# Kernel optimization log

Hardware: AMD Instinct MI355X
Metric: run time of the kernel (lower is better)

## Reference

```python
import jax, jax.numpy as jnp
import numpy as np

SLOPE = 0.01  # torch LeakyReLU default negative_slope

def _leaky(v):
    return jnp.where(v >= 0, v, SLOPE * v)

def _conv3d(x, w, b, stride):
    y = jax.lax.conv_general_dilated(
        x, w, window_strides=(stride, stride, stride), padding='VALID',
        dimension_numbers=('NCDHW', 'OIDHW', 'NCDHW'))
    return y + b[None, :, None, None, None]

def setup_inputs() -> dict:
    key = jax.random.key(0)
    ks = jax.random.split(key, 12)
    s = 0.05  # small init scale to keep exp(L1) numerically sane
    x = jax.random.normal(ks[0], (64, 1, 92, 92, 92), dtype=jnp.float32)
    w1 = jax.random.normal(ks[1], (16, 1, 6, 6, 6), dtype=jnp.float32) * s
    b1 = jnp.zeros((16,), jnp.float32)
    w2 = jax.random.normal(ks[2], (32, 16, 5, 5, 5), dtype=jnp.float32) * s
    b2 = jnp.zeros((32,), jnp.float32)
    w3 = jax.random.normal(ks[3], (48, 32, 5, 5, 5), dtype=jnp.float32) * s
    b3 = jnp.zeros((48,), jnp.float32)
    w4 = jax.random.normal(ks[4], (64, 48, 3, 3, 3), dtype=jnp.float32) * s
    b4 = jnp.zeros((64,), jnp.float32)
    T = jax.random.normal(ks[5], (512, 64 * 16), dtype=jnp.float32) * s
    Wm = jax.random.normal(ks[6], (512 + 64, 1), dtype=jnp.float32) * s
    bm = jnp.zeros((1,), jnp.float32)
    return {'x': x, 'w1': w1, 'b1': b1, 'w2': w2, 'b2': b2, 'w3': w3,
            'b3': b3, 'w4': w4, 'b4': b4, 'T': T, 'Wm': Wm, 'bm': bm}

def reference(x, w1, b1, w2, b2, w3, b3, w4, b4, T, Wm, bm):
    h = _leaky(_conv3d(x, w1, b1, 2))   # [N,16,44,44,44]
    h = _leaky(_conv3d(h, w2, b2, 3))   # [N,32,14,14,14]
    h = _leaky(_conv3d(h, w3, b3, 3))   # [N,48,4,4,4]
    h = _leaky(_conv3d(h, w4, b4, 1))   # [N,64,2,2,2]
    feature = h.reshape(h.shape[0], -1)  # [N,512]
    # minibatch discrimination: M [N,64,16]
    M = (feature @ T).reshape(-1, 64, 16)
    # pairwise L1 over last dim -> [N,N,64]; sum_j exp(.) -> [N,64]
    dist = jnp.sum(jnp.abs(M[:, None, :, :] - M[None, :, :, :]), axis=-1)
    out_T = jnp.sum(jnp.exp(dist), axis=1)
    z = jnp.concatenate([feature, out_T], axis=1) @ Wm + bm
    return jax.nn.sigmoid(z)
```

## Files before the change

kernel.cpp:

```cpp
#include <hip/hip_runtime.h>
#include <hip/hip_bf16.h>
#include <hip/hip_fp16.h>

typedef _Float16 v2h __attribute__((ext_vector_type(2)));
typedef _Float16 v8h __attribute__((ext_vector_type(8)));
typedef __fp16  v2hf __attribute__((ext_vector_type(2)));
typedef float v4f __attribute__((ext_vector_type(4)));

static inline __device__ float leaky(float v) { return v >= 0.f ? v : 0.01f * v; }

static inline __device__ v2h pkrtz(float a, float b) {
    v2hf r = __builtin_amdgcn_cvt_pkrtz(a, b);
    return __builtin_bit_cast(v2h, r);
}

#define W4T_OFF   0
#define H3_OFF    1655808
#define FEAT_OFF  1852416
#define M_OFF     1885184
#define OT_OFF    1950720
#define F16_BASE  1954816
#define WL1_OFF   0
#define BF2_OFF   4608
#define BF3_OFF   81408
#define H2C_OFF   273408
#define H1C_OFF   5893120

__global__ void prep_kernel(const float* __restrict__ w1, const float* __restrict__ w2,
                            const float* __restrict__ w3, const float* __restrict__ w4,
                            float* __restrict__ w4t, _Float16* __restrict__ Bw1,
                            _Float16* __restrict__ Bf2, _Float16* __restrict__ Bf3) {
    int i = blockIdx.x * 256 + threadIdx.x;
    if (i < 4608) {
        int ks = i >> 9, l = (i >> 3) & 63, j = i & 7;
        int oc = l & 15, kg = l >> 4;
        int g = ks * 4 + kg;
        int kz = g / 6, ky = g % 6;
        Bw1[i] = (j < 6) ? (_Float16)w1[oc * 216 + kz * 36 + ky * 6 + j]
                         : (_Float16)0.f;
    } else if (i < 4608 + 76800) {
        int j2 = i - 4608;
        int nt = j2 / 38400, r = j2 % 38400;
        int t = r / 512, l = (r % 512) >> 3, j = r & 7;
        int oc = nt * 16 + (l & 15);
        int k = (l >> 4) * 8 + j;
        int kz = t / 15, ky = (t % 15) / 3, kxp = t % 3;
        int kx = kxp * 2 + (k >= 16 ? 1 : 0);
        int ic = k & 15;
        Bf2[j2] = (kx < 5) ? (_Float16)w2[oc * 2000 + ic * 125 + kz * 25 + ky * 5 + kx]
                           : (_Float16)0.f;
    } else if (i < 4608 + 76800 + 192000) {
        int j3 = i - (4608 + 76800);
        int nt = j3 / 64000, r = j3 % 64000;
        int tap = r / 512, l = (r % 512) >> 3, j = r & 7;
        int oc = nt * 16 + (l & 15);
        int ic = (l >> 4) * 8 + j;
        Bf3[j3] = (_Float16)w3[oc * 4000 + ic * 125 + tap];
    } else {
        int j4 = i - (4608 + 76800 + 192000);
        if (j4 < 82944) {
            int oc = j4 & 63, t = j4 >> 6;
            w4t[j4] = w4[oc * 1296 + t];
        }
    }
}

__global__ __launch_bounds__(256, 2) void conv1_kernel(
    const float* __restrict__ x, const _Float16* __restrict__ Bw1,
    const float* __restrict__ b1, _Float16* __restrict__ h1c, int n0, int NT) {
    __shared__ __align__(16) _Float16 buf[2][13824];
    int tid = threadIdx.x;
    int lane = tid & 63, wv = tid >> 6;
    int col = lane & 15, kg = lane >> 4;

    int t0 = blockIdx.x;
    if (t0 >= NT) return;

    int D_[13], W_[13];
    bool act_[13];
#pragma unroll
    for (int i = 0; i < 13; i++) {
        int u = tid + i * 256;
        act_[i] = (u < 3312);
        int uu = act_[i] ? u : 0;
        int row = uu / 23, c = uu % 23;
        D_[i] = (row / 12) * 8464 + (row % 12) * 92 + 4 * c;
        W_[i] = row * 96 + 4 * c;
    }

    v8h Bv[9];
#pragma unroll
    for (int ks = 0; ks < 9; ks++) Bv[ks] = *(const v8h*)(Bw1 + ks * 512 + lane * 8);
    int offs[9];
#pragma unroll
    for (int ks = 0; ks < 9; ks++) {
        int g = ks * 4 + kg;
        offs[ks] = ((g / 6) * 12 + (g % 6)) * 192;
    }
    float bias = b1[col];

    if (tid < 144) {
        uint2 zz; zz.x = 0u; zz.y = 0u;
        *(uint2*)(&buf[0][tid * 96 + 92]) = zz;
        *(uint2*)(&buf[1][tid * 96 + 92]) = zz;
    }

    {
        int nb = t0 / 121, rr = t0 % 121;
        const float* bp = x + (long)(n0 + nb) * 778688 + (rr / 11) * 8 * 8464 + (rr % 11) * 8 * 92;
        float4 ld[13];
#pragma unroll
        for (int i = 0; i < 13; i++) if (act_[i]) ld[i] = *(const float4*)(bp + D_[i]);
#pragma unroll
        for (int i = 0; i < 13; i++) if (act_[i]) {
            union { v2h h[2]; uint2 u2; } pk;
            pk.h[0] = pkrtz(ld[i].x, ld[i].y);
            pk.h[1] = pkrtz(ld[i].z, ld[i].w);
            *(uint2*)(&buf[0][W_[i]]) = pk.u2;
        }
    }
    __syncthreads();

    int cur = 0;
    int stride = gridDim.x;
    for (int t = t0; t < NT; t += stride) {
        int tn = t + stride;
        bool hn = tn < NT;
        float4 ld[13];
        if (hn) {
            int nb = tn / 121, rr = tn % 121;
            const float* bp = x + (long)(n0 + nb) * 778688 + (rr / 11) * 8 * 8464 + (rr % 11) * 8 * 92;
#pragma unroll
            for (int i = 0; i < 13; i++) if (act_[i]) ld[i] = *(const float4*)(bp + D_[i]);
        }
        __builtin_amdgcn_sched_barrier(0);

        {
            int nb = t / 121, rr = t % 121;
            int zq = rr / 11, yt = rr % 11;
            const uint* lds32 = (const uint*)&buf[cur][0];
            int z = zq * 4 + wv;
            for (int yy = 0; yy < 4; yy++) {
#pragma unroll
                for (int xt = 0; xt < 3; xt++) {
                    int xo_base = (xt == 2) ? 28 : (xt << 4);
                    int base_byte = (24 * wv + 2 * yy) * 192 + (xo_base + col) * 4;
                    v4f acc = {0.f, 0.f, 0.f, 0.f};
#pragma unroll
                    for (int ks = 0; ks < 9; ks++) {
                        int di = (base_byte + offs[ks]) >> 2;
                        union { uint u[4]; v8h h; } A;
                        A.u[0] = lds32[di + 0];
                        A.u[1] = lds32[di + 1];
                        A.u[2] = lds32[di + 2];
                        A.u[3] = lds32[di + 3];
                        acc = __builtin_amdgcn_mfma_f32_16x16x32_f16(A.h, Bv[ks], acc, 0, 0, 0);
                    }
                    int y = yt * 4 + yy;
                    long obase = ((long)((nb * 44 + z) * 44 + y) * 44 + xo_base + kg * 4) * 16 + col;
#pragma unroll
                    for (int reg = 0; reg < 4; reg++) {
                        h1c[obase + reg * 16] = (_Float16)leaky(acc[reg] + bias);
                    }
                }
            }
        }

        if (hn) {
            _Float16* wb = &buf[cur ^ 1][0];
#pragma unroll
            for (int i = 0; i < 13; i++) if (act_[i]) {
                union { v2h h[2]; uint2 u2; } pk;
                pk.h[0] = pkrtz(ld[i].x, ld[i].y);
                pk.h[1] = pkrtz(ld[i].z, ld[i].w);
                *(uint2*)(wb + W_[i]) = pk.u2;
            }
        }
        __syncthreads();
        cur ^= 1;
    }
}

__global__ __launch_bounds__(256) void conv2_kernel(
    const _Float16* __restrict__ h1c, const _Float16* __restrict__ Bf2,
    const float* __restrict__ b2, _Float16* __restrict__ h2c, int n0, int mlimit) {
    int tid = threadIdx.x;
    int lane = tid & 63, wv = tid >> 6;
    int nwg = gridDim.x;
    int orig = blockIdx.x;
    int xcd = orig & 7, lid = orig >> 3;
    int q = nwg >> 3, r = nwg & 7;
    int swz = (xcd < r ? xcd * (q + 1) : r * (q + 1) + (xcd - r) * q) + lid;
    int t0 = (swz * 4 + wv) * 4;
    int col = lane & 15, kgrp = lane >> 4;
    int par = kgrp >> 1, ico = (kgrp & 1) * 8;

    int base[4];
    bool valid[4];
#pragma unroll
    for (int i = 0; i < 4; i++) {
        int m = (t0 + i) * 16 + col;
        valid[i] = m < mlimit;
        int mm = valid[i] ? m : 0;
        int nl = mm / 2744, rm = mm % 2744;
        int z = rm / 196; rm %= 196;
        int y = rm / 14, xx = rm % 14;
        base[i] = nl * 1362944 + z * 3 * 30976 + y * 3 * 704 + xx * 3 * 16 + ico + par * 16;
    }

    v4f acc[4][2];
#pragma unroll
    for (int i = 0; i < 4; i++)
#pragma unroll
        for (int nt = 0; nt < 2; nt++) acc[i][nt] = (v4f){0.f, 0.f, 0.f, 0.f};

    int t = 0;
    for (int kz = 0; kz < 5; kz++) {
        for (int ky = 0; ky < 5; ky++) {
#pragma unroll
            for (int kxp = 0; kxp < 3; kxp++, t++) {
                int d = kz * 30976 + ky * 704 + kxp * 32;
                v8h B0 = *(const v8h*)(Bf2 + t * 512 + lane * 8);
                v8h B1 = *(const v8h*)(Bf2 + (75 + t) * 512 + lane * 8);
                v8h A0 = *(const v8h*)(h1c + base[0] + d);
                v8h A1 = *(const v8h*)(h1c + base[1] + d);
                v8h A2 = *(const v8h*)(h1c + base[2] + d);
                v8h A3 = *(const v8h*)(h1c + base[3] + d);
                acc[0][0] = __builtin_amdgcn_mfma_f32_16x16x32_f16(A0, B0, acc[0][0], 0, 0, 0);
                acc[0][1] = __builtin_amdgcn_mfma_f32_16x16x32_f16(A0, B1, acc[0][1], 0, 0, 0);
                acc[1][0] = __builtin_amdgcn_mfma_f32_16x16x32_f16(A1, B0, acc[1][0], 0, 0, 0);
                acc[1][1] = __builtin_amdgcn_mfma_f32_16x16x32_f16(A1, B1, acc[1][1], 0, 0, 0);
                acc[2][0] = __builtin_amdgcn_mfma_f32_16x16x32_f16(A2, B0, acc[2][0], 0, 0, 0);
                acc[2][1] = __builtin_amdgcn_mfma_f32_16x16x32_f16(A2, B1, acc[2][1], 0, 0, 0);
                acc[3][0] = __builtin_amdgcn_mfma_f32_16x16x32_f16(A3, B0, acc[3][0], 0, 0, 0);
                acc[3][1] = __builtin_amdgcn_mfma_f32_16x16x32_f16(A3, B1, acc[3][1], 0, 0, 0);
            }
        }
    }

#pragma unroll
    for (int i = 0; i < 4; i++) {
        if (!valid[i]) continue;
#pragma unroll
        for (int nt = 0; nt < 2; nt++) {
            int oc = nt * 16 + col;
            float bb = b2[oc];
#pragma unroll
            for (int reg = 0; reg < 4; reg++) {
                int mlocal = (t0 + i) * 16 + kgrp * 4 + reg;
                float vv = leaky(acc[i][nt][reg] + bb);
                h2c[(long)(n0 * 2744 + mlocal) * 32 + oc] = (_Float16)vv;
            }
        }
    }
}

__global__ __launch_bounds__(256) void conv3_kernel(
    const _Float16* __restrict__ h2c, const _Float16* __restrict__ Bf3,
    const float* __restrict__ b3, float* __restrict__ h3) {
    __shared__ float part[3][64][13];
    int tid = threadIdx.x;
    int lane = tid & 63, wv = tid >> 6;
    int mt = blockIdx.x;
    int col = lane & 15, kgrp = lane >> 4;
    int m = mt * 16 + col;
    int n = m >> 6, pos = m & 63;
    int z = pos >> 4, y = (pos >> 2) & 3, xx = pos & 3;
    int base = (n * 2744 + z * 3 * 196 + y * 3 * 14 + xx * 3) * 32 + kgrp * 8;

    v4f acc[3];
#pragma unroll
    for (int nt = 0; nt < 3; nt++) acc[nt] = (v4f){0.f, 0.f, 0.f, 0.f};

    int tap0 = wv * 32;
    int tap1 = tap0 + 32 < 125 ? tap0 + 32 : 125;
    for (int tap = tap0; tap < tap1; tap++) {
        int kz = tap / 25, rr = tap % 25, ky = rr / 5, kx = rr % 5;
        int d = (kz * 196 + ky * 14 + kx) * 32;
        v8h A  = *(const v8h*)(h2c + base + d);
        v8h B0 = *(const v8h*)(Bf3 + tap * 512 + lane * 8);
        v8h B1 = *(const v8h*)(Bf3 + (125 + tap) * 512 + lane * 8);
        v8h B2 = *(const v8h*)(Bf3 + (250 + tap) * 512 + lane * 8);
        acc[0] = __builtin_amdgcn_mfma_f32_16x16x32_f16(A, B0, acc[0], 0, 0, 0);
        acc[1] = __builtin_amdgcn_mfma_f32_16x16x32_f16(A, B1, acc[1], 0, 0, 0);
        acc[2] = __builtin_amdgcn_mfma_f32_16x16x32_f16(A, B2, acc[2], 0, 0, 0);
    }

    if (wv > 0) {
#pragma unroll
        for (int nt = 0; nt < 3; nt++)
#pragma unroll
            for (int reg = 0; reg < 4; reg++)
                part[wv - 1][lane][nt * 4 + reg] = acc[nt][reg];
    }
    __syncthreads();
    if (wv == 0) {
#pragma unroll
        for (int w = 0; w < 3; w++)
#pragma unroll
            for (int nt = 0; nt < 3; nt++)
#pragma unroll
                for (int reg = 0; reg < 4; reg++)
                    acc[nt][reg] += part[w][lane][nt * 4 + reg];
#pragma unroll
        for (int nt = 0; nt < 3; nt++) {
            int oc = nt * 16 + col;
            float bb = b3[oc];
#pragma unroll
            for (int reg = 0; reg < 4; reg++) {
                int md = mt * 16 + kgrp * 4 + reg;
                h3[((md >> 6) * 48 + oc) * 64 + (md & 63)] = leaky(acc[nt][reg] + bb);
            }
        }
    }
}

__global__ void conv4_kernel(const float* __restrict__ h3, const float* __restrict__ w4t,
                             const float* __restrict__ b4, float* __restrict__ feat) {
    int o = blockIdx.x * 128 + threadIdx.x;
    int pos = o & 7;
    int oc  = (o >> 3) & 63;
    int n   = o >> 9;
    int px = pos & 1, py = (pos >> 1) & 1, pz = pos >> 2;
    const float* xn = h3 + (long)n * 48 * 64;
    float acc = 0.f;
    for (int ic = 0; ic < 48; ic++) {
        const float* xc = xn + ic * 64;
        int tb = ic * 27;
#pragma unroll
        for (int kz = 0; kz < 3; kz++)
#pragma unroll
            for (int ky = 0; ky < 3; ky++)
#pragma unroll
                for (int kx = 0; kx < 3; kx++) {
                    float v = xc[(pz + kz) * 16 + (py + ky) * 4 + (px + kx)];
                    acc += v * w4t[(tb + (kz * 3 + ky) * 3 + kx) * 64 + oc];
                }
    }
    feat[o] = leaky(acc + b4[oc]);
}

__global__ void m_kernel(const float* __restrict__ feat, const float* __restrict__ T,
                         float* __restrict__ M) {
    int o = blockIdx.x * 256 + threadIdx.x;
    int col = o & 1023;
    int n   = o >> 10;
    const float* fr = feat + n * 512;
    float acc = 0.f;
#pragma unroll 4
    for (int f = 0; f < 512; f++) acc += fr[f] * T[f * 1024 + col];
    M[o] = acc;
}

__global__ void outt_kernel(const float* __restrict__ M, float* __restrict__ oT) {
    __shared__ float part[3][64];
    int i = blockIdx.x;
    int tid = threadIdx.x;
    int k = tid & 63, jq = tid >> 6;
    float mi[16];
    const float4* Mi = (const float4*)(M + i * 1024 + k * 16);
#pragma unroll
    for (int q = 0; q < 4; q++) {
        float4 a = Mi[q];
        mi[q*4+0] = a.x; mi[q*4+1] = a.y; mi[q*4+2] = a.z; mi[q*4+3] = a.w;
    }
    float s = 0.f;
    for (int j = jq * 16; j < jq * 16 + 16; j++) {
        const float4* Mj = (const float4*)(M + j * 1024 + k * 16);
        float d = 0.f;
#pragma unroll
        for (int q = 0; q < 4; q++) {
            float4 a = Mj[q];
            d += fabsf(mi[q*4+0]-a.x) + fabsf(mi[q*4+1]-a.y) + fabsf(mi[q*4+2]-a.z) + fabsf(mi[q*4+3]-a.w);
        }
        s += __expf(d);
    }
    if (jq > 0) part[jq - 1][k] = s;
    __syncthreads();
    if (jq == 0) {
        s += part[0][k] + part[1][k] + part[2][k];
        oT[i * 64 + k] = s;
    }
}

__global__ void final_kernel(const float* __restrict__ feat, const float* __restrict__ oT,
                             const float* __restrict__ Wm, const float* __restrict__ bm,
                             float* __restrict__ out) {
    int i = blockIdx.x;
    int lane = threadIdx.x;
    const float* fr = feat + i * 512;
    float z = 0.f;
#pragma unroll
    for (int q = 0; q < 8; q++) z += fr[lane + q * 64] * Wm[lane + q * 64];
    z += oT[i * 64 + lane] * Wm[512 + lane];
#pragma unroll
    for (int off = 32; off > 0; off >>= 1) z += __shfl_down(z, off);
    if (lane == 0) out[i] = 1.f / (1.f + __expf(-(z + bm[0])));
}

extern "C" void kernel_launch(void* const* d_in, const int* in_sizes, int n_in,
                              void* d_out, int out_size, void* d_ws, size_t ws_size,
                              hipStream_t stream) {
    const float* x  = (const float*)d_in[0];
    const float* w1 = (const float*)d_in[1];
    const float* b1 = (const float*)d_in[2];
    const float* w2 = (const float*)d_in[3];
    const float* b2 = (const float*)d_in[4];
    const float* w3 = (const float*)d_in[5];
    const float* b3 = (const float*)d_in[6];
    const float* w4 = (const float*)d_in[7];
    const float* b4 = (const float*)d_in[8];
    const float* T  = (const float*)d_in[9];
    const float* Wm = (const float*)d_in[10];
    const float* bm = (const float*)d_in[11];

    float* ws   = (float*)d_ws;
    float* w4t  = ws + W4T_OFF;
    float* h3   = ws + H3_OFF;
    float* feat = ws + FEAT_OFF;
    float* Mb   = ws + M_OFF;
    float* oT   = ws + OT_OFF;
    _Float16* f16b = (_Float16*)(ws + F16_BASE);
    _Float16* Bw1  = f16b + WL1_OFF;
    _Float16* Bf2  = f16b + BF2_OFF;
    _Float16* Bf3  = f16b + BF3_OFF;
    _Float16* h2c  = f16b + H2C_OFF;
    _Float16* h1c  = f16b + H1C_OFF;

    prep_kernel<<<1392, 256, 0, stream>>>(w1, w2, w3, w4, w4t, Bw1, Bf2, Bf3);

    size_t fixed_bytes = (size_t)F16_BASE * 4 + (size_t)H1C_OFF * 2;
    int NB;
    if (ws_size >= fixed_bytes + (64ll * 1362944 + 64) * 2) NB = 64;
    else if (ws_size >= fixed_bytes + (16ll * 1362944 + 64) * 2) NB = 16;
    else NB = 8;

    for (int n0 = 0; n0 < 64; n0 += NB) {
        conv1_kernel<<<512, 256, 0, stream>>>(x, Bw1, b1, h1c, n0, NB * 121);
        int mlimit = NB * 2744;
        int blocks2 = (mlimit + 255) / 256;
        conv2_kernel<<<blocks2, 256, 0, stream>>>(h1c, Bf2, b2, h2c, n0, mlimit);
    }
    conv3_kernel<<<256, 256, 0, stream>>>(h2c, Bf3, b3, h3);
    conv4_kernel<<<256, 128, 0, stream>>>(h3, w4t, b4, feat);
    m_kernel<<<256, 256, 0, stream>>>(feat, T, Mb);
    outt_kernel<<<64, 256, 0, stream>>>(Mb, oT);
    final_kernel<<<64, 64, 0, stream>>>(feat, oT, Wm, bm, (float*)d_out);
}
```

Measured before the change: 582.6 us.

## Retune work split across conv1-conv4 kernels and vectorize conv4 weights

```diff
diff --git a/kernel.cpp b/kernel.cpp
--- a/kernel.cpp
+++ b/kernel.cpp
@@ -14,7 +14,7 @@
     return __builtin_bit_cast(v2h, r);
 }
 
-#define W4T_OFF   0
+#define W4S_OFF   0
 #define H3_OFF    1655808
 #define FEAT_OFF  1852416
 #define M_OFF     1885184
@@ -28,7 +28,7 @@
 
 __global__ void prep_kernel(const float* __restrict__ w1, const float* __restrict__ w2,
                             const float* __restrict__ w3, const float* __restrict__ w4,
-                            float* __restrict__ w4t, _Float16* __restrict__ Bw1,
+                            float* __restrict__ w4s, _Float16* __restrict__ Bw1,
                             _Float16* __restrict__ Bf2, _Float16* __restrict__ Bf3) {
     int i = blockIdx.x * 256 + threadIdx.x;
     if (i < 4608) {
@@ -58,29 +58,30 @@
         Bf3[j3] = (_Float16)w3[oc * 4000 + ic * 125 + tap];
     } else {
         int j4 = i - (4608 + 76800 + 192000);
-        if (j4 < 82944) {
-            int oc = j4 & 63, t = j4 >> 6;
-            w4t[j4] = w4[oc * 1296 + t];
-        }
-    }
-}
-
-__global__ __launch_bounds__(256, 2) void conv1_kernel(
+        if (j4 < 110592) {
+            int kx = j4 & 3, r = (j4 >> 2) % 9, ic = (j4 >> 2) / 9 % 48, oc = j4 / 1728;
+            w4s[j4] = (kx < 3) ? w4[oc * 1296 + ic * 27 + r * 3 + kx] : 0.f;
+        }
+    }
+}
+
+__global__ __launch_bounds__(512, 4) void conv1_kernel(
     const float* __restrict__ x, const _Float16* __restrict__ Bw1,
     const float* __restrict__ b1, _Float16* __restrict__ h1c, int n0, int NT) {
     __shared__ __align__(16) _Float16 buf[2][13824];
     int tid = threadIdx.x;
     int lane = tid & 63, wv = tid >> 6;
     int col = lane & 15, kg = lane >> 4;
+    int zl = wv & 3, yh = wv >> 2;
 
     int t0 = blockIdx.x;
     if (t0 >= NT) return;
 
-    int D_[13], W_[13];
-    bool act_[13];
-#pragma unroll
-    for (int i = 0; i < 13; i++) {
-        int u = tid + i * 256;
+    int D_[7], W_[7];
+    bool act_[7];
+#pragma unroll
+    for (int i = 0; i < 7; i++) {
+        int u = tid + i * 512;
         act_[i] = (u < 3312);
         int uu = act_[i] ? u : 0;
         int row = uu / 23, c = uu % 23;
@@ -108,11 +109,11 @@
     {
         int nb = t0 / 121, rr = t0 % 121;
         const float* bp = x + (long)(n0 + nb) * 778688 + (rr / 11) * 8 * 8464 + (rr % 11) * 8 * 92;
-        float4 ld[13];
-#pragma unroll
-        for (int i = 0; i < 13; i++) if (act_[i]) ld[i] = *(const float4*)(bp + D_[i]);
-#pragma unroll
-        for (int i = 0; i < 13; i++) if (act_[i]) {
+        float4 ld[7];
+#pragma unroll
+        for (int i = 0; i < 7; i++) if (act_[i]) ld[i] = *(const float4*)(bp + D_[i]);
+#pragma unroll
+        for (int i = 0; i < 7; i++) if (act_[i]) {
             union { v2h h[2]; uint2 u2; } pk;
             pk.h[0] = pkrtz(ld[i].x, ld[i].y);
             pk.h[1] = pkrtz(ld[i].z, ld[i].w);
@@ -126,12 +127,12 @@
     for (int t = t0; t < NT; t += stride) {
         int tn = t + stride;
         bool hn = tn < NT;
-        float4 ld[13];
+        float4 ld[7];
         if (hn) {
             int nb = tn / 121, rr = tn % 121;
             const float* bp = x + (long)(n0 + nb) * 778688 + (rr / 11) * 8 * 8464 + (rr % 11) * 8 * 92;
 #pragma unroll
-            for (int i = 0; i < 13; i++) if (act_[i]) ld[i] = *(const float4*)(bp + D_[i]);
+            for (int i = 0; i < 7; i++) if (act_[i]) ld[i] = *(const float4*)(bp + D_[i]);
         }
         __builtin_amdgcn_sched_barrier(0);
 
@@ -139,12 +140,14 @@
             int nb = t / 121, rr = t % 121;
             int zq = rr / 11, yt = rr % 11;
             const uint* lds32 = (const uint*)&buf[cur][0];
-            int z = zq * 4 + wv;
-            for (int yy = 0; yy < 4; yy++) {
+            int z = zq * 4 + zl;
+#pragma unroll
+            for (int yy = 0; yy < 2; yy++) {
+                int yl = yh * 2 + yy;
 #pragma unroll
                 for (int xt = 0; xt < 3; xt++) {
                     int xo_base = (xt == 2) ? 28 : (xt << 4);
-                    int base_byte = (24 * wv + 2 * yy) * 192 + (xo_base + col) * 4;
+                    int base_byte = (24 * zl + 2 * yl) * 192 + (xo_base + col) * 4;
                     v4f acc = {0.f, 0.f, 0.f, 0.f};
 #pragma unroll
                     for (int ks = 0; ks < 9; ks++) {
@@ -156,7 +159,7 @@
                         A.u[3] = lds32[di + 3];
                         acc = __builtin_amdgcn_mfma_f32_16x16x32_f16(A.h, Bv[ks], acc, 0, 0, 0);
                     }
-                    int y = yt * 4 + yy;
+                    int y = yt * 4 + yl;
                     long obase = ((long)((nb * 44 + z) * 44 + y) * 44 + xo_base + kg * 4) * 16 + col;
 #pragma unroll
                     for (int reg = 0; reg < 4; reg++) {
@@ -169,7 +172,7 @@
         if (hn) {
             _Float16* wb = &buf[cur ^ 1][0];
 #pragma unroll
-            for (int i = 0; i < 13; i++) if (act_[i]) {
+            for (int i = 0; i < 7; i++) if (act_[i]) {
                 union { v2h h[2]; uint2 u2; } pk;
                 pk.h[0] = pkrtz(ld[i].x, ld[i].y);
                 pk.h[1] = pkrtz(ld[i].z, ld[i].w);
@@ -191,14 +194,14 @@
     int xcd = orig & 7, lid = orig >> 3;
     int q = nwg >> 3, r = nwg & 7;
     int swz = (xcd < r ? xcd * (q + 1) : r * (q + 1) + (xcd - r) * q) + lid;
-    int t0 = (swz * 4 + wv) * 4;
+    int t0 = (swz * 4 + wv) * 2;
     int col = lane & 15, kgrp = lane >> 4;
     int par = kgrp >> 1, ico = (kgrp & 1) * 8;
 
-    int base[4];
-    bool valid[4];
-#pragma unroll
-    for (int i = 0; i < 4; i++) {
+    int base[2];
+    bool valid[2];
+#pragma unroll
+    for (int i = 0; i < 2; i++) {
         int m = (t0 + i) * 16 + col;
         valid[i] = m < mlimit;
         int mm = valid[i] ? m : 0;
@@ -208,9 +211,9 @@
         base[i] = nl * 1362944 + z * 3 * 30976 + y * 3 * 704 + xx * 3 * 16 + ico + par * 16;
     }
 
-    v4f acc[4][2];
-#pragma unroll
-    for (int i = 0; i < 4; i++)
+    v4f acc[2][2];
+#pragma unroll
+    for (int i = 0; i < 2; i++)
 #pragma unroll
         for (int nt = 0; nt < 2; nt++) acc[i][nt] = (v4f){0.f, 0.f, 0.f, 0.f};
 
@@ -224,22 +227,16 @@
                 v8h B1 = *(const v8h*)(Bf2 + (75 + t) * 512 + lane * 8);
                 v8h A0 = *(const v8h*)(h1c + base[0] + d);
                 v8h A1 = *(const v8h*)(h1c + base[1] + d);
-                v8h A2 = *(const v8h*)(h1c + base[2] + d);
-                v8h A3 = *(const v8h*)(h1c + base[3] + d);
                 acc[0][0] = __builtin_amdgcn_mfma_f32_16x16x32_f16(A0, B0, acc[0][0], 0, 0, 0);
                 acc[0][1] = __builtin_amdgcn_mfma_f32_16x16x32_f16(A0, B1, acc[0][1], 0, 0, 0);
                 acc[1][0] = __builtin_amdgcn_mfma_f32_16x16x32_f16(A1, B0, acc[1][0], 0, 0, 0);
                 acc[1][1] = __builtin_amdgcn_mfma_f32_16x16x32_f16(A1, B1, acc[1][1], 0, 0, 0);
-                acc[2][0] = __builtin_amdgcn_mfma_f32_16x16x32_f16(A2, B0, acc[2][0], 0, 0, 0);
-                acc[2][1] = __builtin_amdgcn_mfma_f32_16x16x32_f16(A2, B1, acc[2][1], 0, 0, 0);
-                acc[3][0] = __builtin_amdgcn_mfma_f32_16x16x32_f16(A3, B0, acc[3][0], 0, 0, 0);
-                acc[3][1] = __builtin_amdgcn_mfma_f32_16x16x32_f16(A3, B1, acc[3][1], 0, 0, 0);
-            }
-        }
-    }
-
-#pragma unroll
-    for (int i = 0; i < 4; i++) {
+            }
+        }
+    }
+
+#pragma unroll
+    for (int i = 0; i < 2; i++) {
         if (!valid[i]) continue;
 #pragma unroll
         for (int nt = 0; nt < 2; nt++) {
@@ -255,10 +252,10 @@
     }
 }
 
-__global__ __launch_bounds__(256) void conv3_kernel(
+__global__ __launch_bounds__(512) void conv3_kernel(
     const _Float16* __restrict__ h2c, const _Float16* __restrict__ Bf3,
     const float* __restrict__ b3, float* __restrict__ h3) {
-    __shared__ float part[3][64][13];
+    __shared__ float part[7][64][13];
     int tid = threadIdx.x;
     int lane = tid & 63, wv = tid >> 6;
     int mt = blockIdx.x;
@@ -272,8 +269,8 @@
 #pragma unroll
     for (int nt = 0; nt < 3; nt++) acc[nt] = (v4f){0.f, 0.f, 0.f, 0.f};
 
-    int tap0 = wv * 32;
-    int tap1 = tap0 + 32 < 125 ? tap0 + 32 : 125;
+    int tap0 = wv * 16;
+    int tap1 = tap0 + 16 < 125 ? tap0 + 16 : 125;
     for (int tap = tap0; tap < tap1; tap++) {
         int kz = tap / 25, rr = tap % 25, ky = rr / 5, kx = rr % 5;
         int d = (kz * 196 + ky * 14 + kx) * 32;
@@ -296,7 +293,7 @@
     __syncthreads();
     if (wv == 0) {
 #pragma unroll
-        for (int w = 0; w < 3; w++)
+        for (int w = 0; w < 7; w++)
 #pragma unroll
             for (int nt = 0; nt < 3; nt++)
 #pragma unroll
@@ -315,27 +312,29 @@
     }
 }
 
-__global__ void conv4_kernel(const float* __restrict__ h3, const float* __restrict__ w4t,
+__global__ void conv4_kernel(const float* __restrict__ h3, const float* __restrict__ w4s,
                              const float* __restrict__ b4, float* __restrict__ feat) {
-    int o = blockIdx.x * 128 + threadIdx.x;
+    int o = blockIdx.x * 64 + threadIdx.x;
     int pos = o & 7;
     int oc  = (o >> 3) & 63;
     int n   = o >> 9;
     int px = pos & 1, py = (pos >> 1) & 1, pz = pos >> 2;
     const float* xn = h3 + (long)n * 48 * 64;
+    const float4* wp = (const float4*)(w4s + oc * 1728);
     float acc = 0.f;
     for (int ic = 0; ic < 48; ic++) {
         const float* xc = xn + ic * 64;
-        int tb = ic * 27;
 #pragma unroll
         for (int kz = 0; kz < 3; kz++)
 #pragma unroll
-            for (int ky = 0; ky < 3; ky++)
-#pragma unroll
-                for (int kx = 0; kx < 3; kx++) {
-                    float v = xc[(pz + kz) * 16 + (py + ky) * 4 + (px + kx)];
-                    acc += v * w4t[(tb + (kz * 3 + ky) * 3 + kx) * 64 + oc];
-                }
+            for (int ky = 0; ky < 3; ky++) {
+                float4 xq = *(const float4*)(xc + (pz + kz) * 16 + (py + ky) * 4);
+                float4 wq = wp[ic * 9 + kz * 3 + ky];
+                float a0 = px ? xq.y : xq.x;
+                float a1 = px ? xq.z : xq.y;
+                float a2 = px ? xq.w : xq.z;
+                acc += a0 * wq.x + a1 * wq.y + a2 * wq.z;
+            }
     }
     feat[o] = leaky(acc + b4[oc]);
 }
@@ -415,7 +414,7 @@
     const float* bm = (const float*)d_in[11];
 
     float* ws   = (float*)d_ws;
-    float* w4t  = ws + W4T_OFF;
+    float* w4s  = ws + W4S_OFF;
     float* h3   = ws + H3_OFF;
     float* feat = ws + FEAT_OFF;
     float* Mb   = ws + M_OFF;
@@ -427,7 +426,7 @@
     _Float16* h2c  = f16b + H2C_OFF;
     _Float16* h1c  = f16b + H1C_OFF;
 
-    prep_kernel<<<1392, 256, 0, stream>>>(w1, w2, w3, w4, w4t, Bw1, Bf2, Bf3);
+    prep_kernel<<<1500, 256, 0, stream>>>(w1, w2, w3, w4, w4s, Bw1, Bf2, Bf3);
 
     size_t fixed_bytes = (size_t)F16_BASE * 4 + (size_t)H1C_OFF * 2;
     int NB;
@@ -436,13 +435,13 @@
     else NB = 8;
 
     for (int n0 = 0; n0 < 64; n0 += NB) {
-        conv1_kernel<<<512, 256, 0, stream>>>(x, Bw1, b1, h1c, n0, NB * 121);
+        conv1_kernel<<<512, 512, 0, stream>>>(x, Bw1, b1, h1c, n0, NB * 121);
         int mlimit = NB * 2744;
-        int blocks2 = (mlimit + 255) / 256;
+        int blocks2 = (mlimit + 127) / 128;
         conv2_kernel<<<blocks2, 256, 0, stream>>>(h1c, Bf2, b2, h2c, n0, mlimit);
     }
-    conv3_kernel<<<256, 256, 0, stream>>>(h2c, Bf3, b3, h3);
-    conv4_kernel<<<256, 128, 0, stream>>>(h3, w4t, b4, feat);
+    conv3_kernel<<<256, 512, 0, stream>>>(h2c, Bf3, b3, h3);
+    conv4_kernel<<<512, 64, 0, stream>>>(h3, w4s, b4, feat);
     m_kernel<<<256, 256, 0, stream>>>(feat, T, Mb);
     outt_kernel<<<64, 256, 0, stream>>>(Mb, oT);
     final_kernel<<<64, 64, 0, stream>>>(feat, oT, Wm, bm, (float*)d_out);
```

Measured after the change: 594.7 us. +2.1%, slower.
